# Kernel optimization log

Measured on AMD Instinct MI355X. Metric: run time of the kernel, lower is better.

## Reference

```python
import jax, jax.numpy as jnp
import numpy as np

NH, NKV, HD = 32, 8, 64
GROUPS = NH // NKV
NLAYERS, FREQ = 30, 3
NSLOTS = 1 + NLAYERS // FREQ  # 11
LAYER_IDX = 0
TOPK = 128
KB_SCALE = 100.0
PAD = -3.3895313892515355e+38  # torch.finfo(bfloat16).min


def rotate_half(x):
    d = x.shape[-1] // 2
    return jnp.concatenate([-x[..., d:], x[..., :d]], axis=-1)


def apply_rope(x, cos, sin):
    # x: (B, H, S, D); cos/sin: (B, S, D)
    return x * cos[:, None] + rotate_half(x) * sin[:, None]


def setup_inputs() -> dict:
    key = jax.random.key(0)
    ks = jax.random.split(key, 10)
    B, S, H = 2, 1024, 2048
    KBL = 400
    hidden_states = jax.random.normal(ks[0], (B, S, H), jnp.float32)
    # rotary embeddings (LlamaRotaryEmbedding, theta=10000)
    pos = jnp.arange(S, dtype=jnp.float32)
    inv_freq = 1.0 / (10000.0 ** (jnp.arange(0, HD, 2, dtype=jnp.float32) / HD))
    freqs = pos[:, None] * inv_freq[None, :]
    emb = jnp.concatenate([freqs, freqs], axis=-1)  # (S, HD)
    cos = jnp.broadcast_to(jnp.cos(emb)[None], (B, S, HD)).astype(jnp.float32)
    sin = jnp.broadcast_to(jnp.sin(emb)[None], (B, S, HD)).astype(jnp.float32)
    # additive causal mask (B,1,S,S)
    causal = jnp.where(jnp.tril(jnp.ones((S, S), jnp.bool_)), 0.0, PAD).astype(jnp.float32)
    attention_mask = jnp.broadcast_to(causal[None, None], (B, 1, S, S))
    kb_keys = jax.random.normal(ks[1], (KBL, NSLOTS * NH * HD), jnp.float32) * 0.5
    kb_values = jax.random.normal(ks[2], (KBL, NSLOTS * NH * HD), jnp.float32) * 0.5
    s = 0.02
    Wq = jax.random.normal(ks[3], (NH * HD, H), jnp.float32) * s
    Wq2 = jax.random.normal(ks[4], (NH * HD, H), jnp.float32) * s
    Wk = jax.random.normal(ks[5], (NKV * HD, H), jnp.float32) * s
    Wv = jax.random.normal(ks[6], (NKV * HD, H), jnp.float32) * s
    Wo = jax.random.normal(ks[7], (H, NH * HD), jnp.float32) * s
    return {"hidden_states": hidden_states, "cos": cos, "sin": sin,
            "attention_mask": attention_mask, "kb_keys": kb_keys, "kb_values": kb_values,
            "Wq": Wq, "Wq2": Wq2, "Wk": Wk, "Wv": Wv, "Wo": Wo}


def reference(hidden_states, cos, sin, attention_mask, kb_keys, kb_values, Wq, Wq2, Wk, Wv, Wo):
    B, S, H = hidden_states.shape
    scale = 1.0 / jnp.sqrt(jnp.float32(HD))

    # projections (attention_bias=False)
    q = (hidden_states @ Wq.T).reshape(B, S, NH, HD).transpose(0, 2, 1, 3)
    q2 = (hidden_states @ Wq2.T).reshape(B, S, NH, HD).transpose(0, 2, 1, 3)
    k = (hidden_states @ Wk.T).reshape(B, S, NKV, HD).transpose(0, 2, 1, 3)
    v = (hidden_states @ Wv.T).reshape(B, S, NKV, HD).transpose(0, 2, 1, 3)

    q = apply_rope(q, cos, sin)
    k = apply_rope(k, cos, sin)

    # repeat_kv (GQA)
    k = jnp.repeat(k, GROUPS, axis=1)  # (B, NH, S, HD)
    v = jnp.repeat(v, GROUPS, axis=1)

    # KB slot select (layer_idx % freq == 0, kb_idx = layer_idx // freq = 0)
    KBL = kb_keys.shape[0]
    kb_idx = LAYER_IDX // FREQ
    kbk = kb_keys.reshape(KBL, NSLOTS, NH * HD)[:, kb_idx].reshape(KBL, NH, HD).transpose(1, 0, 2)
    kbv = kb_values.reshape(KBL, NSLOTS, NH * HD)[:, kb_idx].reshape(KBL, NH, HD).transpose(1, 0, 2)
    kbk = jnp.broadcast_to(kbk[None], (B, NH, KBL, HD))
    kbv = jnp.broadcast_to(kbv[None], (B, NH, KBL, HD))

    # dynamic_sparsify: prune_key_value
    aw_kb = jnp.einsum('bhsd,bhkd->bhsk', q2, kbk) * scale  # (B,NH,S,KBL)
    scores = aw_kb.sum(axis=(1, 2))  # (B, KBL)
    top_idx = jax.lax.stop_gradient(jax.lax.top_k(scores, TOPK)[1])  # (B, TOPK)
    idx = jnp.broadcast_to(top_idx[:, None, :, None], (B, NH, TOPK, HD))
    kbk_g = jax.lax.stop_gradient(jnp.take_along_axis(kbk, idx, axis=2))  # gather under no_grad
    kbv_g = jax.lax.stop_gradient(jnp.take_along_axis(kbv, idx, axis=2))
    aw2 = aw_kb[..., :TOPK]  # source slices (not gathers) the first topk columns

    key_states = jnp.concatenate([kbk_g, k], axis=2)  # (B,NH,TOPK+S,HD)
    value_states = jnp.concatenate([kbv_g, v], axis=2)

    # KB attention mask block
    padding = jnp.all(attention_mask < 0, axis=-1, keepdims=True)  # (B,1,S,1)
    kb_mask = jnp.where(padding, PAD, 0.0).astype(attention_mask.dtype)
    kb_mask = jnp.broadcast_to(kb_mask, (B, 1, S, TOPK))
    mask = jnp.concatenate([kb_mask, attention_mask], axis=-1)  # (B,1,S,TOPK+S)

    aw = jnp.einsum('bhsd,bhkd->bhsk', q, key_states) * scale
    # seperate_query_head: replace KB block with q2-based scores (with kb scale shift)
    aw_seq = aw[..., TOPK:]
    aw2 = aw2 - np.log(TOPK) + np.log(KB_SCALE)
    aw = jnp.concatenate([aw2, aw_seq], axis=-1)

    aw = aw + mask[:, :, :, :key_states.shape[2]]
    aw = jax.nn.softmax(aw.astype(jnp.float32), axis=-1).astype(q.dtype)

    attn = jnp.einsum('bhsk,bhkd->bhsd', aw, value_states)  # (B,NH,S,HD)
    attn = attn.transpose(0, 2, 1, 3).reshape(B, S, NH * HD)
    return attn @ Wo.T
```

## Files before the change

kernel.cpp:

```cpp
#include <hip/hip_runtime.h>
#include <hip/hip_bf16.h>
#include <math.h>

#define NH 32
#define NKV 8
#define HD 64
#define NSLOTS 11
#define TOPK 128
#define KBROW (NSLOTS * NH * HD)
#define PADF (-3.3895313892515355e+38f)
#define C0F  (-0.24686007793152578f)
#define SCALE 0.125f
#define HCH 32

typedef __attribute__((ext_vector_type(8))) __bf16 bf16x8;
typedef __attribute__((ext_vector_type(8))) unsigned short u16x8;
typedef __attribute__((ext_vector_type(4))) float f32x4;

#define GLDS16(gp, lp)                                                        \
  __builtin_amdgcn_global_load_lds(                                           \
      (__attribute__((address_space(1))) void*)(gp),                          \
      (__attribute__((address_space(3))) void*)(lp), 16, 0, 0)

__device__ __forceinline__ unsigned short f2bf(float f) {
  unsigned int u = __float_as_uint(f);
  u = (u + 0x7fffu + ((u >> 16) & 1u)) >> 16;
  return (unsigned short)u;
}

__device__ __forceinline__ int swz(int row, int chunk) {
  return row * 128 + ((chunk ^ (row & 7)) << 4);
}

__global__ void f2bf_all(const float* __restrict__ s0, const float* __restrict__ s1,
                         const float* __restrict__ s2, const float* __restrict__ s3,
                         const float* __restrict__ s4,
                         int n0, int n1, int n2, int n3, int n4_,
                         unsigned short* __restrict__ out) {
  int i = blockIdx.x * blockDim.x + threadIdx.x;
  int j = i;
  const float* src;
  if (j < n0) src = s0;
  else { j -= n0; if (j < n1) src = s1;
  else { j -= n1; if (j < n2) src = s2;
  else { j -= n2; if (j < n3) src = s3;
  else { j -= n3; if (j >= n4_) return; src = s4; }}}}
  float4 v = ((const float4*)src)[j];
  ushort4 o = {f2bf(v.x), f2bf(v.y), f2bf(v.z), f2bf(v.w)};
  ((ushort4*)out)[i] = o;
}

__global__ __launch_bounds__(256) void gemm_nt_splitk(
    const unsigned short* __restrict__ A, const unsigned short* __restrict__ B,
    float* __restrict__ C0, float* __restrict__ C1, int M, int N, int K) {
  __shared__ unsigned short ldsA[128 * 32];
  __shared__ unsigned short ldsB[128 * 32];
  const int t = threadIdx.x;
  const int l = t & 63, w = t >> 6;
  const int wr = w >> 1, wc = w & 1;
  const int lr = l & 15;
  const int kb = (l >> 4) * 16;
  const int bm = blockIdx.y * 128, bn = blockIdx.x * 128;
  float* C = blockIdx.z ? C1 : C0;
  const int k0base = blockIdx.z * (K >> 1);
  const int kend = k0base + (K >> 1);

  f32x4 acc[4][4] = {};

  for (int k0 = k0base; k0 < kend; k0 += 32) {
    __syncthreads();
#pragma unroll
    for (int it = 0; it < 2; ++it) {
      int s = it * 256 + t;
      int row = s >> 2, cs = (s & 3) * 8;
      GLDS16(A + (size_t)(bm + row) * K + k0 + cs,
             (char*)ldsA + (it * 4 + w) * 1024);
      GLDS16(B + (size_t)(bn + row) * K + k0 + cs,
             (char*)ldsB + (it * 4 + w) * 1024);
    }
    __syncthreads();

    bf16x8 a[4], b[4];
#pragma unroll
    for (int m = 0; m < 4; ++m)
      a[m] = *(const bf16x8*)((const char*)ldsA +
                              (wr * 64 + m * 16 + lr) * 64 + kb);
#pragma unroll
    for (int n = 0; n < 4; ++n)
      b[n] = *(const bf16x8*)((const char*)ldsB +
                              (wc * 64 + n * 16 + lr) * 64 + kb);
#pragma unroll
    for (int m = 0; m < 4; ++m)
#pragma unroll
      for (int n = 0; n < 4; ++n)
        acc[m][n] =
            __builtin_amdgcn_mfma_f32_16x16x32_bf16(a[m], b[n], acc[m][n], 0, 0, 0);
  }

#pragma unroll
  for (int m = 0; m < 4; ++m)
#pragma unroll
    for (int n = 0; n < 4; ++n) {
      int rbase = bm + wr * 64 + m * 16 + ((l >> 4) << 2);
      int cbase = bn + wc * 64 + n * 16 + lr;
#pragma unroll
      for (int j = 0; j < 4; ++j)
        C[(size_t)(rbase + j) * N + cbase] = acc[m][n][j];
    }
}

__global__ void add2_kernel(const float* __restrict__ a,
                            const float* __restrict__ b,
                            float* __restrict__ o, int n4) {
  int i = blockIdx.x * blockDim.x + threadIdx.x;
  if (i >= n4) return;
  float4 x = ((const float4*)a)[i], y = ((const float4*)b)[i];
  ((float4*)o)[i] = make_float4(x.x + y.x, x.y + y.y, x.z + y.z, x.w + y.w);
}

__global__ __launch_bounds__(512) void gemm_proj8(
    const unsigned short* __restrict__ A,
    const unsigned short* __restrict__ Wall,
    const float* __restrict__ cosb, const float* __restrict__ sinb,
    unsigned short* __restrict__ qbf, unsigned short* __restrict__ q2bf,
    unsigned short* __restrict__ kbf, unsigned short* __restrict__ vTb,
    int M, int K, int S) {
  __shared__ char lds[131072];
  const int t = threadIdx.x;
  const int w = t >> 6;
  const int wm = w >> 2, wn = w & 3;
  const int l = t & 63;
  const int li = l & 15, lg4 = l >> 4;
  const int bm = blockIdx.y * 256, bn = blockIdx.x * 256;
  const int NK = K >> 6;

  f32x4 acc[8][4] = {};

#define STAGE_UNIT(kt1, nb, u)                                                \
  {                                                                           \
    const int slice_ = (u) >> 1;                                              \
    const unsigned short* mat_ = ((u) & 1) ? Wall : A;                        \
    const int tb_ = ((u) & 1) ? bn : bm;                                      \
    char* base_ = lds + (nb) * 65536 + (((u) & 1) ? 32768 : 0) +              \
                  slice_ * 16384;                                             \
    _Pragma("unroll")                                                         \
    for (int i_ = 0; i_ < 2; ++i_) {                                          \
      int ss_ = i_ * 512 + t;                                                 \
      int row_ = ss_ >> 2, cc_ = ss_ & 3;                                     \
      int chunk_ = cc_ ^ ((row_ >> 1) & 3);                                   \
      GLDS16(mat_ + (size_t)(tb_ + row_) * K + (kt1) * 64 + slice_ * 32 +     \
                 chunk_ * 8,                                                  \
             base_ + i_ * 8192 + w * 1024);                                   \
    }                                                                         \
  }

  STAGE_UNIT(0, 0, 0); STAGE_UNIT(0, 0, 1);
  STAGE_UNIT(0, 0, 2); STAGE_UNIT(0, 0, 3);
  asm volatile("s_waitcnt vmcnt(4)" ::: "memory");
  asm volatile("s_barrier" ::: "memory");

  for (int kt = 0; kt < NK; ++kt) {
    const int cur = kt & 1;
    const bool stg = (kt + 1 < NK);
    char* curA = lds + cur * 65536;
    char* curB = curA + 32768;
#pragma unroll
    for (int kk = 0; kk < 2; ++kk) {
      bf16x8 bfr[4], af_a[4], af_b[4];
#pragma unroll
      for (int n = 0; n < 4; ++n) {
        int row = wn * 64 + n * 16 + li;
        bfr[n] = *(const bf16x8*)(curB + kk * 16384 + row * 64 +
                                  ((lg4 ^ ((row >> 1) & 3)) << 4));
      }
#pragma unroll
      for (int mi = 0; mi < 4; ++mi) {
        int row = wm * 128 + mi * 16 + li;
        af_a[mi] = *(const bf16x8*)(curA + kk * 16384 + row * 64 +
                                    ((lg4 ^ ((row >> 1) & 3)) << 4));
      }
      if (stg) STAGE_UNIT(kt + 1, cur ^ 1, kk * 2)
#pragma unroll
      for (int mi = 0; mi < 4; ++mi) {
        int row = wm * 128 + (4 + mi) * 16 + li;
        af_b[mi] = *(const bf16x8*)(curA + kk * 16384 + row * 64 +
                                    ((lg4 ^ ((row >> 1) & 3)) << 4));
      }
#pragma unroll
      for (int mi = 0; mi < 4; ++mi)
#pragma unroll
        for (int n = 0; n < 4; ++n)
          acc[mi][n] = __builtin_amdgcn_mfma_f32_16x16x32_bf16(
              af_a[mi], bfr[n], acc[mi][n], 0, 0, 0);
      if (stg) STAGE_UNIT(kt + 1, cur ^ 1, kk * 2 + 1)
#pragma unroll
      for (int mi = 0; mi < 4; ++mi)
#pragma unroll
        for (int n = 0; n < 4; ++n)
          acc[4 + mi][n] = __builtin_amdgcn_mfma_f32_16x16x32_bf16(
              af_b[mi], bfr[n], acc[4 + mi][n], 0, 0, 0);
      if (kk == 0) {
        if (kt == NK - 1) asm volatile("s_waitcnt vmcnt(0)" ::: "memory");
        else              asm volatile("s_waitcnt vmcnt(4)" ::: "memory");
        asm volatile("s_barrier" ::: "memory");
      } else {
        if (stg) {
          asm volatile("s_waitcnt vmcnt(4)" ::: "memory");
          asm volatile("s_barrier" ::: "memory");
        }
      }
    }
  }
#undef STAGE_UNIT

  const int seg = bn;
#pragma unroll
  for (int m = 0; m < 8; ++m) {
    const int row0 = bm + wm * 128 + m * 16 + lg4 * 4;
    if (seg < 2048 || (seg >= 4096 && seg < 4608)) {
      const bool isq = seg < 2048;
#pragma unroll
      for (int j = 0; j < 4; ++j) {
        int row = row0 + j;
        const float* cr = cosb + (size_t)row * 64;
        const float* sr = sinb + (size_t)row * 64;
        float c0 = cr[li], c1 = cr[16 + li], c2 = cr[32 + li], c3 = cr[48 + li];
        float sa = sr[li], sb = sr[16 + li], sc_ = sr[32 + li], sd = sr[48 + li];
        float x0 = acc[m][0][j], x1 = acc[m][1][j];
        float x2 = acc[m][2][j], x3 = acc[m][3][j];
        float y0 = x0 * c0 - x2 * sa;
        float y1 = x1 * c1 - x3 * sb;
        float y2 = x2 * c2 + x0 * sc_;
        float y3 = x3 * c3 + x1 * sd;
        if (isq) {
          size_t ro = (size_t)row * 2048 + bn + wn * 64 + li;
          qbf[ro] = f2bf(y0); qbf[ro + 16] = f2bf(y1);
          qbf[ro + 32] = f2bf(y2); qbf[ro + 48] = f2bf(y3);
        } else {
          size_t ro = (size_t)row * 512 + (bn - 4096) + wn * 64 + li;
          kbf[ro] = f2bf(y0); kbf[ro + 16] = f2bf(y1);
          kbf[ro + 32] = f2bf(y2); kbf[ro + 48] = f2bf(y3);
        }
      }
    } else if (seg < 4096) {
#pragma unroll
      for (int n = 0; n < 4; ++n) {
        int col = bn - 2048 + wn * 64 + n * 16 + li;
#pragma unroll
        for (int j = 0; j < 4; ++j)
          q2bf[(size_t)(row0 + j) * 2048 + col] = f2bf(acc[m][n][j]);
      }
    } else {
      int b_ = row0 / S, s = row0 % S;
#pragma unroll
      for (int n = 0; n < 4; ++n) {
        int col = (bn - 4608) + wn * 64 + n * 16 + li;
        int gg = col >> 6, d = col & 63;
        ushort4 o = {f2bf(acc[m][n][0]), f2bf(acc[m][n][1]),
                     f2bf(acc[m][n][2]), f2bf(acc[m][n][3])};
        *(ushort4*)&vTb[(((size_t)b_ * NKV + gg) * 64 + d) * S + s] = o;
      }
    }
  }
}

__global__ void kbkh_kernel(const float* __restrict__ kbk,
                            unsigned short* __restrict__ out) {
  int i = blockIdx.x * blockDim.x + threadIdx.x;
  if (i >= 128 * 512) return;
  int j = i >> 9, c4 = (i & 511) * 4;
  float4 v = *(const float4*)&kbk[(size_t)j * KBROW + c4];
  ushort4 o = {f2bf(v.x), f2bf(v.y), f2bf(v.z), f2bf(v.w)};
  *(ushort4*)&out[(size_t)j * 2048 + c4] = o;
}

__global__ __launch_bounds__(256) void kbvgt_kernel(
    const float* __restrict__ kbv, const int* __restrict__ topi,
    unsigned short* __restrict__ kbvgT, int B) {
  int h = blockIdx.x % NH, b = blockIdx.x / NH;
  __shared__ unsigned short gt[128][72];
  __shared__ int lidx[TOPK];
  int t = threadIdx.x;
  if (t < TOPK) lidx[t] = topi[b * TOPK + t];
  __syncthreads();
#pragma unroll
  for (int it = 0; it < 8; ++it) {
    int slot = it * 256 + t;
    int j = slot >> 4, d4 = (slot & 15) * 4;
    float4 v = *(const float4*)&kbv[(size_t)lidx[j] * KBROW + h * 64 + d4];
    gt[j][d4] = f2bf(v.x); gt[j][d4 + 1] = f2bf(v.y);
    gt[j][d4 + 2] = f2bf(v.z); gt[j][d4 + 3] = f2bf(v.w);
  }
  __syncthreads();
#pragma unroll
  for (int it = 0; it < 4; ++it) {
    int slot = it * 256 + t;
    int d = slot >> 4, j8 = (slot & 15) * 8;
    u16x8 o;
#pragma unroll
    for (int j = 0; j < 8; ++j) o[j] = gt[j8 + j][d];
    *(u16x8*)&kbvgT[(((size_t)b * NH + h) * 64 + d) * 128 + j8] = o;
  }
}

__global__ __launch_bounds__(256) void hsum1_kernel(
    const float* __restrict__ hidden, double* __restrict__ part,
    unsigned short* __restrict__ hbf, int B, int S, int H) {
  const int nhb = H >> 8;
  int hb = blockIdx.x % nhb;
  int ch = (blockIdx.x / nhb) % HCH;
  int b  = blockIdx.x / (nhb * HCH);
  int c  = hb * 256 + threadIdx.x;
  int rows = S / HCH;
  size_t base = ((size_t)b * S + (size_t)ch * rows) * H + c;
  const float* p = hidden + base;
  double acc = 0.0;
  for (int s = 0; s < rows; ++s) {
    float v = p[(size_t)s * H];
    acc += (double)v;
    hbf[base + (size_t)s * H] = f2bf(v);
  }
  part[((size_t)b * HCH + ch) * H + c] = acc;
}

__global__ void hsum2_kernel(const double* __restrict__ part,
                             float* __restrict__ Hsum, int B, int H) {
  int idx = blockIdx.x * blockDim.x + threadIdx.x;
  if (idx >= B * H) return;
  int b = idx / H, c = idx % H;
  const double* p = part + (size_t)b * HCH * H + c;
  double acc = 0.0;
#pragma unroll
  for (int ch = 0; ch < HCH; ++ch) acc += p[(size_t)ch * H];
  Hsum[idx] = (float)acc;
}

__global__ void qs_kernel(const float* __restrict__ Hsum,
                          const float* __restrict__ Wq2,
                          float* __restrict__ Qs, int B, int H) {
  int task = (blockIdx.x * blockDim.x + threadIdx.x) >> 6;
  int lane = threadIdx.x & 63;
  if (task >= B * NH * HD) return;
  int b = task / (NH * HD), c = task % (NH * HD);
  const float* hs = Hsum + (size_t)b * H;
  const float* wr = Wq2 + (size_t)c * H;
  double acc = 0.0;
  for (int k = lane; k < H; k += 64) acc += (double)hs[k] * (double)wr[k];
#pragma unroll
  for (int off = 32; off; off >>= 1) acc += __shfl_xor(acc, off);
  if (lane == 0) Qs[task] = (float)acc;
}

__global__ void scores_kernel(const float* __restrict__ Qs,
                              const float* __restrict__ kbk,
                              float* __restrict__ scores, int B, int KBL) {
  int task = (blockIdx.x * blockDim.x + threadIdx.x) >> 6;
  int lane = threadIdx.x & 63;
  if (task >= B * KBL) return;
  int b = task / KBL, l = task % KBL;
  const float* kr = kbk + (size_t)l * KBROW;
  const float* qd = Qs + (size_t)b * NH * HD;
  double acc = 0.0;
  for (int c = lane; c < NH * HD; c += 64) acc += (double)qd[c] * (double)kr[c];
#pragma unroll
  for (int off = 32; off; off >>= 1) acc += __shfl_xor(acc, off);
  if (lane == 0) scores[task] = (float)(0.125 * acc);
}

__global__ __launch_bounds__(256) void topk_kernel(
    const float* __restrict__ scores, int* __restrict__ top_idx, int KBL) {
  __shared__ float ls[512];
  int b = blockIdx.x, t = threadIdx.x;
  for (int i = t; i < KBL; i += 256) ls[i] = scores[(size_t)b * KBL + i];
  __syncthreads();
  for (int l = t; l < KBL; l += 256) {
    float sl = ls[l];
    int rank = 0;
    for (int j = 0; j < KBL; ++j) {
      float sj = ls[j];
      rank += (sj > sl || (sj == sl && j < l)) ? 1 : 0;
    }
    if (rank < TOPK) top_idx[b * TOPK + rank] = l;
  }
}

__global__ void padflag_kernel(const float* __restrict__ mask,
                               int* __restrict__ flags, int BS, int S) {
  int w = (blockIdx.x * blockDim.x + threadIdx.x) >> 6;
  int lane = threadIdx.x & 63;
  if (w >= BS) return;
  const float* row = mask + (size_t)w * S;
  bool ok = true;
  for (int j = lane; j < S; j += 64) ok = ok && (row[j] < 0.f);
  int allv = __all(ok ? 1 : 0);
  if (lane == 0) flags[w] = allv;
}

__device__ __forceinline__ void load_chunk(
    int ch, int t, int b, int h, int g, int S,
    const unsigned short* __restrict__ kbf, const unsigned short* __restrict__ vTb,
    const unsigned short* __restrict__ kbkh, const unsigned short* __restrict__ kbvgT,
    bf16x8* st) {
  bool iskb = ch < 2;
  int j0 = iskb ? ch * 64 : (ch - 2) * 64;
#pragma unroll
  for (int it = 0; it < 4; ++it) {
    int slot = it * 256 + t;
    int tile = slot >> 9, row = (slot >> 3) & 63, ck = slot & 7;
    const unsigned short* src;
    if (tile == 0)
      src = iskb ? kbkh + (size_t)(j0 + row) * 2048 + h * 64 + ck * 8
                 : kbf + (size_t)(b * S + j0 + row) * 512 + g * 64 + ck * 8;
    else
      src = iskb ? kbvgT + (((size_t)b * NH + h) * 64 + row) * 128 + j0 + ck * 8
                 : vTb + (((size_t)b * NKV + g) * 64 + row) * (size_t)S + j0 + ck * 8;
    st[it] = *(const bf16x8*)src;
  }
}

__device__ __forceinline__ void attn_step(
    const char* cbuf, char* ptw, const int* padfb, const bf16x8* aq,
    bool iskb, int j0, int s0, int w, int li, int lg4,
    float* m_, float* l_, f32x4* acc) {
  f32x4 cc[4];
  __builtin_amdgcn_s_setprio(1);
#pragma unroll
  for (int cb = 0; cb < 4; ++cb) {
    bf16x8 b0 = *(const bf16x8*)(cbuf + swz(cb * 16 + li, lg4));
    bf16x8 b1 = *(const bf16x8*)(cbuf + swz(cb * 16 + li, 4 + lg4));
    f32x4 z = {};
    z = __builtin_amdgcn_mfma_f32_16x16x32_bf16(aq[0], b0, z, 0, 0, 0);
    z = __builtin_amdgcn_mfma_f32_16x16x32_bf16(aq[1], b1, z, 0, 0, 0);
    cc[cb] = z;
  }
  __builtin_amdgcn_s_setprio(0);

  float lgv[4][4];
#pragma unroll
  for (int cb = 0; cb < 4; ++cb)
#pragma unroll
    for (int j = 0; j < 4; ++j) {
      float v = SCALE * cc[cb][j];
      if (iskb) {
        v += C0F + (padfb[w * 16 + lg4 * 4 + j] ? PADF : 0.f);
      } else {
        int key = j0 + cb * 16 + li;
        int srow = s0 + w * 16 + lg4 * 4 + j;
        v += (key <= srow) ? 0.f : PADF;
      }
      lgv[cb][j] = v;
    }
#pragma unroll
  for (int j = 0; j < 4; ++j) {
    float rmax = fmaxf(fmaxf(lgv[0][j], lgv[1][j]), fmaxf(lgv[2][j], lgv[3][j]));
#pragma unroll
    for (int off = 8; off; off >>= 1) rmax = fmaxf(rmax, __shfl_xor(rmax, off));
    float mn = fmaxf(m_[j], rmax);
    float fs = __expf(m_[j] - mn);
    float csum = 0.f;
#pragma unroll
    for (int cb = 0; cb < 4; ++cb) {
      float pv = __expf(lgv[cb][j] - mn);
      csum += pv;
      int key = cb * 16 + li;
      int rloc = lg4 * 4 + j;
      *(unsigned short*)(ptw + swz(rloc, key >> 3) + ((key & 7) << 1)) = f2bf(pv);
    }
#pragma unroll
    for (int off = 8; off; off >>= 1) csum += __shfl_xor(csum, off);
    m_[j] = mn;
    l_[j] = l_[j] * fs + csum;
#pragma unroll
    for (int db = 0; db < 4; ++db) acc[db][j] *= fs;
  }

  bf16x8 pa0 = *(const bf16x8*)(ptw + swz(li, lg4));
  bf16x8 pa1 = *(const bf16x8*)(ptw + swz(li, 4 + lg4));
  __builtin_amdgcn_s_setprio(1);
#pragma unroll
  for (int db = 0; db < 4; ++db) {
    bf16x8 bv0 = *(const bf16x8*)(cbuf + 8192 + swz(db * 16 + li, lg4));
    bf16x8 bv1 = *(const bf16x8*)(cbuf + 8192 + swz(db * 16 + li, 4 + lg4));
    acc[db] = __builtin_amdgcn_mfma_f32_16x16x32_bf16(pa0, bv0, acc[db], 0, 0, 0);
    acc[db] = __builtin_amdgcn_mfma_f32_16x16x32_bf16(pa1, bv1, acc[db], 0, 0, 0);
  }
  __builtin_amdgcn_s_setprio(0);
}

__global__ __launch_bounds__(256) void attn_mfma(
    const unsigned short* __restrict__ qbf,
    const unsigned short* __restrict__ q2bf,
    const unsigned short* __restrict__ kbf,
    const unsigned short* __restrict__ vTb,
    const unsigned short* __restrict__ kbkh,
    const unsigned short* __restrict__ kbvgT,
    const int* __restrict__ padflag,
    unsigned short* __restrict__ attnbf,
    int B, int S) {
  const int nst = S >> 6;
  const int npair = (nst + 1) >> 1;
  const int p = blockIdx.x % npair;
  const int h = (blockIdx.x / npair) % NH;
  const int b = blockIdx.x / (npair * NH);
  const int stA = p, stB = nst - 1 - p;
  const bool hasB = (stB != stA);
  const int s0A = stA * 64, s0B = stB * 64;
  const int g = h / (NH / NKV);

  __shared__ unsigned short smem[2][8192];
  __shared__ unsigned short pt[4][1024];
  __shared__ int padf[128];

  const int t = threadIdx.x;
  const int w = t >> 6;
  const int li = t & 15;
  const int lg4 = (t & 63) >> 4;

  const int nch = 2 + stB + 1;

  bf16x8 st[4];
  load_chunk(0, t, b, h, g, S, kbf, vTb, kbkh, kbvgT, st);

  bf16x8 aq0A[2], aq2A[2], aq0B[2], aq2B[2];
  {
    size_t rowA = (size_t)(b * S + s0A + w * 16 + li) * (NH * HD);
    size_t rowB = (size_t)(b * S + s0B + w * 16 + li) * (NH * HD);
#pragma unroll
    for (int kc = 0; kc < 2; ++kc) {
      size_t o = h * 64 + kc * 32 + lg4 * 8;
      aq0A[kc] = *(const bf16x8*)(qbf + rowA + o);
      aq2A[kc] = *(const bf16x8*)(q2bf + rowA + o);
      aq0B[kc] = *(const bf16x8*)(qbf + rowB + o);
      aq2B[kc] = *(const bf16x8*)(q2bf + rowB + o);
    }
  }
  if (t < 64) padf[t] = padflag[b * S + s0A + t];
  else if (t < 128) padf[t] = padflag[b * S + s0B + (t - 64)];

#pragma unroll
  for (int it = 0; it < 4; ++it) {
    int slot = it * 256 + t;
    int tile = slot >> 9, row = (slot >> 3) & 63, ck = slot & 7;
    *(bf16x8*)((char*)smem[0] + tile * 8192 + swz(row, ck)) = st[it];
  }
  load_chunk(1, t, b, h, g, S, kbf, vTb, kbkh, kbvgT, st);
  __syncthreads();

  float mA[4] = {-3.4e38f, -3.4e38f, -3.4e38f, -3.4e38f};
  float mB[4] = {-3.4e38f, -3.4e38f, -3.4e38f, -3.4e38f};
  float lA[4] = {}, lB[4] = {};
  f32x4 accA[4] = {}, accB[4] = {};

  for (int ch = 0; ch < nch; ++ch) {
    const bool iskb = ch < 2;
    const int j0 = iskb ? ch * 64 : (ch - 2) * 64;
    if (ch + 1 < nch) {
      char* nb = (char*)smem[(ch + 1) & 1];
#pragma unroll
      for (int it = 0; it < 4; ++it) {
        int slot = it * 256 + t;
        int tile = slot >> 9, row = (slot >> 3) & 63, ck = slot & 7;
        *(bf16x8*)(nb + tile * 8192 + swz(row, ck)) = st[it];
      }
      if (ch + 2 < nch)
        load_chunk(ch + 2, t, b, h, g, S, kbf, vTb, kbkh, kbvgT, st);
    }
    const char* cb = (const char*)smem[ch & 1];
    if (iskb || (ch - 2) <= stA)
      attn_step(cb, (char*)pt[w], padf, iskb ? aq2A : aq0A,
                iskb, j0, s0A, w, li, lg4, mA, lA, accA);
    if (hasB)
      attn_step(cb, (char*)pt[w], padf + 64, iskb ? aq2B : aq0B,
                iskb, j0, s0B, w, li, lg4, mB, lB, accB);
    __syncthreads();
  }

#pragma unroll
  for (int j = 0; j < 4; ++j) {
    float inv = 1.f / lA[j];
    size_t o = (size_t)(b * S + s0A + w * 16 + lg4 * 4 + j) * (NH * HD) + h * 64 + li;
#pragma unroll
    for (int db = 0; db < 4; ++db) attnbf[o + db * 16] = f2bf(accA[db][j] * inv);
  }
  if (hasB) {
#pragma unroll
    for (int j = 0; j < 4; ++j) {
      float inv = 1.f / lB[j];
      size_t o = (size_t)(b * S + s0B + w * 16 + lg4 * 4 + j) * (NH * HD) + h * 64 + li;
#pragma unroll
      for (int db = 0; db < 4; ++db) attnbf[o + db * 16] = f2bf(accB[db][j] * inv);
    }
  }
}

extern "C" void kernel_launch(void* const* d_in, const int* in_sizes, int n_in,
                              void* d_out, int out_size, void* d_ws, size_t ws_size,
                              hipStream_t stream) {
  const float* hidden = (const float*)d_in[0];
  const float* cosb   = (const float*)d_in[1];
  const float* sinb   = (const float*)d_in[2];
  const float* mask   = (const float*)d_in[3];
  const float* kbk    = (const float*)d_in[4];
  const float* kbv    = (const float*)d_in[5];
  const float* Wq     = (const float*)d_in[6];
  const float* Wq2    = (const float*)d_in[7];
  const float* Wk     = (const float*)d_in[8];
  const float* Wv     = (const float*)d_in[9];
  const float* Wo     = (const float*)d_in[10];
  float* out = (float*)d_out;

  const int H   = in_sizes[6] / (NH * HD);
  const int KBL = in_sizes[4] / KBROW;
  const long long BSll = (long long)in_sizes[0] / H;
  const int S = (int)((long long)in_sizes[3] / BSll);
  const int B = (int)(BSll / S);
  const int BS = B * S;
  const int NQ = NH * HD;
  const int NKVD = NKV * HD;
  const int NTOT = NQ + NQ + NKVD + NKVD;

  float* ws = (float*)d_ws;
  size_t off = 0;
  double* hpart = (double*)(ws + off); off += (size_t)B * HCH * H * 2;
  float* Hsum = ws + off; off += (size_t)B * H;
  float* Qs   = ws + off; off += (size_t)B * NQ;
  float* sc   = ws + off; off += (size_t)B * KBL;
  int* topi   = (int*)(ws + off); off += (size_t)B * TOPK;
  int* padfl  = (int*)(ws + off); off += (size_t)BS;
  unsigned short* hbf    = (unsigned short*)(ws + off); off += (size_t)BS * H / 2;
  unsigned short* wall   = (unsigned short*)(ws + off); off += (size_t)NTOT * H / 2;
  unsigned short* wobf   = (unsigned short*)(ws + off); off += (size_t)H * NQ / 2;
  unsigned short* attnbf = (unsigned short*)(ws + off); off += (size_t)BS * NQ / 2;
  unsigned short* qbf    = (unsigned short*)(ws + off); off += (size_t)BS * NQ / 2;
  unsigned short* q2bf   = (unsigned short*)(ws + off); off += (size_t)BS * NQ / 2;
  unsigned short* kbf    = (unsigned short*)(ws + off); off += (size_t)BS * NKVD / 2;
  unsigned short* vTb    = (unsigned short*)(ws + off); off += (size_t)BS * NKVD / 2;
  unsigned short* kbkh   = (unsigned short*)(ws + off); off += (size_t)128 * NQ / 2;
  unsigned short* kbvgT  = (unsigned short*)(ws + off); off += (size_t)B * NH * HD * TOPK / 2;
  float* c0 = (float*)qbf;
  float* c1 = (float*)wall;
  (void)ws_size; (void)n_in; (void)out_size;

  {
    int n1 = NQ * H / 4, n2 = NQ * H / 4;
    int n3 = NKVD * H / 4, n4_ = NKVD * H / 4, n5 = H * NQ / 4;
    int ntot = n1 + n2 + n3 + n4_ + n5;
    f2bf_all<<<(ntot + 255) / 256, 256, 0, stream>>>(
        Wq, Wq2, Wk, Wv, Wo, n1, n2, n3, n4_, n5, wall);
  }

  hsum1_kernel<<<B * HCH * (H / 256), 256, 0, stream>>>(hidden, hpart, hbf, B, S, H);

  gemm_proj8<<<dim3(NTOT / 256, BS / 256), 512, 0, stream>>>(
      hbf, wall, cosb, sinb, qbf, q2bf, kbf, vTb, BS, H, S);

  hsum2_kernel<<<(B * H + 255) / 256, 256, 0, stream>>>(hpart, Hsum, B, H);
  qs_kernel<<<(B * NQ * 64 + 255) / 256, 256, 0, stream>>>(Hsum, Wq2, Qs, B, H);
  scores_kernel<<<(B * KBL * 64 + 255) / 256, 256, 0, stream>>>(Qs, kbk, sc, B, KBL);
  topk_kernel<<<B, 256, 0, stream>>>(sc, topi, KBL);
  padflag_kernel<<<(BS * 64 + 255) / 256, 256, 0, stream>>>(mask, padfl, BS, S);

  kbkh_kernel<<<(128 * 512 + 255) / 256, 256, 0, stream>>>(kbk, kbkh);
  kbvgt_kernel<<<B * NH, 256, 0, stream>>>(kbv, topi, kbvgT, B);

  {
    int nst = S / 64;
    int npair = (nst + 1) / 2;
    attn_mfma<<<B * NH * npair, 256, 0, stream>>>(
        qbf, q2bf, kbf, vTb, kbkh, kbvgT, padfl, attnbf, B, S);
  }

  gemm_nt_splitk<<<dim3(H / 128, BS / 128, 2), 256, 0, stream>>>(
      attnbf, wobf, c0, c1, BS, H, NQ);
  add2_kernel<<<(BS * H / 4 + 255) / 256, 256, 0, stream>>>(c0, c1, out, BS * H / 4);
}
```

Baseline: 247.6 us.

## Split projection GEMM across 16 waves with 64x64 per-wave tiles

```diff
diff --git a/kernel.cpp b/kernel.cpp
--- a/kernel.cpp
+++ b/kernel.cpp
@@ -118,7 +118,7 @@
   ((float4*)o)[i] = make_float4(x.x + y.x, x.y + y.y, x.z + y.z, x.w + y.w);
 }
 
-__global__ __launch_bounds__(512) void gemm_proj8(
+__global__ __launch_bounds__(1024) void gemm_proj8(
     const unsigned short* __restrict__ A,
     const unsigned short* __restrict__ Wall,
     const float* __restrict__ cosb, const float* __restrict__ sinb,
@@ -134,7 +134,7 @@
   const int bm = blockIdx.y * 256, bn = blockIdx.x * 256;
   const int NK = K >> 6;
 
-  f32x4 acc[8][4] = {};
+  f32x4 acc[4][4] = {};
 
 #define STAGE_UNIT(kt1, nb, u)                                                \
   {                                                                           \
@@ -143,20 +143,16 @@
     const int tb_ = ((u) & 1) ? bn : bm;                                      \
     char* base_ = lds + (nb) * 65536 + (((u) & 1) ? 32768 : 0) +              \
                   slice_ * 16384;                                             \
-    _Pragma("unroll")                                                         \
-    for (int i_ = 0; i_ < 2; ++i_) {                                          \
-      int ss_ = i_ * 512 + t;                                                 \
-      int row_ = ss_ >> 2, cc_ = ss_ & 3;                                     \
-      int chunk_ = cc_ ^ ((row_ >> 1) & 3);                                   \
-      GLDS16(mat_ + (size_t)(tb_ + row_) * K + (kt1) * 64 + slice_ * 32 +     \
-                 chunk_ * 8,                                                  \
-             base_ + i_ * 8192 + w * 1024);                                   \
-    }                                                                         \
+    int row_ = t >> 2, cc_ = t & 3;                                           \
+    int chunk_ = cc_ ^ ((row_ >> 1) & 3);                                     \
+    GLDS16(mat_ + (size_t)(tb_ + row_) * K + (kt1) * 64 + slice_ * 32 +       \
+               chunk_ * 8,                                                    \
+           base_ + w * 1024);                                                 \
   }
 
   STAGE_UNIT(0, 0, 0); STAGE_UNIT(0, 0, 1);
   STAGE_UNIT(0, 0, 2); STAGE_UNIT(0, 0, 3);
-  asm volatile("s_waitcnt vmcnt(4)" ::: "memory");
+  asm volatile("s_waitcnt vmcnt(2)" ::: "memory");
   asm volatile("s_barrier" ::: "memory");
 
   for (int kt = 0; kt < NK; ++kt) {
@@ -166,7 +162,7 @@
     char* curB = curA + 32768;
 #pragma unroll
     for (int kk = 0; kk < 2; ++kk) {
-      bf16x8 bfr[4], af_a[4], af_b[4];
+      bf16x8 bfr[4], af[4];
 #pragma unroll
       for (int n = 0; n < 4; ++n) {
         int row = wn * 64 + n * 16 + li;
@@ -175,37 +171,27 @@
       }
 #pragma unroll
       for (int mi = 0; mi < 4; ++mi) {
-        int row = wm * 128 + mi * 16 + li;
-        af_a[mi] = *(const bf16x8*)(curA + kk * 16384 + row * 64 +
-                                    ((lg4 ^ ((row >> 1) & 3)) << 4));
-      }
-      if (stg) STAGE_UNIT(kt + 1, cur ^ 1, kk * 2)
-#pragma unroll
-      for (int mi = 0; mi < 4; ++mi) {
-        int row = wm * 128 + (4 + mi) * 16 + li;
-        af_b[mi] = *(const bf16x8*)(curA + kk * 16384 + row * 64 +
-                                    ((lg4 ^ ((row >> 1) & 3)) << 4));
+        int row = wm * 64 + mi * 16 + li;
+        af[mi] = *(const bf16x8*)(curA + kk * 16384 + row * 64 +
+                                  ((lg4 ^ ((row >> 1) & 3)) << 4));
+      }
+      if (stg) {
+        STAGE_UNIT(kt + 1, cur ^ 1, kk * 2)
+        STAGE_UNIT(kt + 1, cur ^ 1, kk * 2 + 1)
       }
 #pragma unroll
       for (int mi = 0; mi < 4; ++mi)
 #pragma unroll
         for (int n = 0; n < 4; ++n)
           acc[mi][n] = __builtin_amdgcn_mfma_f32_16x16x32_bf16(
-              af_a[mi], bfr[n], acc[mi][n], 0, 0, 0);
-      if (stg) STAGE_UNIT(kt + 1, cur ^ 1, kk * 2 + 1)
-#pragma unroll
-      for (int mi = 0; mi < 4; ++mi)
-#pragma unroll
-        for (int n = 0; n < 4; ++n)
-          acc[4 + mi][n] = __builtin_amdgcn_mfma_f32_16x16x32_bf16(
-              af_b[mi], bfr[n], acc[4 + mi][n], 0, 0, 0);
+              af[mi], bfr[n], acc[mi][n], 0, 0, 0);
       if (kk == 0) {
         if (kt == NK - 1) asm volatile("s_waitcnt vmcnt(0)" ::: "memory");
-        else              asm volatile("s_waitcnt vmcnt(4)" ::: "memory");
+        else              asm volatile("s_waitcnt vmcnt(2)" ::: "memory");
         asm volatile("s_barrier" ::: "memory");
       } else {
         if (stg) {
-          asm volatile("s_waitcnt vmcnt(4)" ::: "memory");
+          asm volatile("s_waitcnt vmcnt(2)" ::: "memory");
           asm volatile("s_barrier" ::: "memory");
         }
       }
@@ -215,8 +201,8 @@
 
   const int seg = bn;
 #pragma unroll
-  for (int m = 0; m < 8; ++m) {
-    const int row0 = bm + wm * 128 + m * 16 + lg4 * 4;
+  for (int m = 0; m < 4; ++m) {
+    const int row0 = bm + wm * 64 + m * 16 + lg4 * 4;
     if (seg < 2048 || (seg >= 4096 && seg < 4608)) {
       const bool isq = seg < 2048;
 #pragma unroll
@@ -651,7 +637,7 @@
 
   hsum1_kernel<<<B * HCH * (H / 256), 256, 0, stream>>>(hidden, hpart, hbf, B, S, H);
 
-  gemm_proj8<<<dim3(NTOT / 256, BS / 256), 512, 0, stream>>>(
+  gemm_proj8<<<dim3(NTOT / 256, BS / 256), 1024, 0, stream>>>(
       hbf, wall, cosb, sinb, qbf, q2bf, kbf, vTb, BS, H, S);
 
   hsum2_kernel<<<(B * H + 255) / 256, 256, 0, stream>>>(hpart, Hsum, B, H);
```

Result: no change. 245.3 us (-0.9%).
